# Kernel tuning notes

Measured on AMD Instinct MI355X. Metric: run time of the kernel, lower is better.

Reference implementation:

```python
import jax, jax.numpy as jnp
import numpy as np

EMBED_DIM = 1024
NUM_HEADS = 16
HEAD_DIM = EMBED_DIM // NUM_HEADS
T_Q = 2048
T_K = 2048
B = 4
NEG_INF = -1e9


def setup_inputs() -> dict:
    key = jax.random.key(0)
    ks = jax.random.split(key, 8)
    q = jax.random.normal(ks[0], (T_Q, B, EMBED_DIM), dtype=jnp.float32)
    k = jax.random.normal(ks[1], (T_K, B, EMBED_DIM), dtype=jnp.float32)
    v = jax.random.normal(ks[2], (T_K, B, EMBED_DIM), dtype=jnp.float32)
    # True = padded key position (masked out)
    key_padding_mask = jax.random.randint(ks[3], (B, T_K), 0, 2).astype(jnp.bool_)
    # torch nn.Linear weights: shape (out, in), y = x @ W^T
    scale = 1.0 / np.sqrt(EMBED_DIM)
    Wq = jax.random.uniform(ks[4], (EMBED_DIM, EMBED_DIM), jnp.float32, -scale, scale)
    Wk = jax.random.uniform(ks[5], (EMBED_DIM, EMBED_DIM), jnp.float32, -scale, scale)
    Wv = jax.random.uniform(ks[6], (EMBED_DIM, EMBED_DIM), jnp.float32, -scale, scale)
    Wo = jax.random.uniform(ks[7], (EMBED_DIM, EMBED_DIM), jnp.float32, -scale, scale)
    return {"q": q, "k": k, "v": v, "key_padding_mask": key_padding_mask,
            "Wq": Wq, "Wk": Wk, "Wv": Wv, "Wo": Wo}


def _proj_split(W, x):
    # x: (T, B, E), W: (E, E) torch layout -> (B, H, T, d_k)
    T = x.shape[0]
    y = jnp.einsum('tbe,fe->tbf', x, W)
    return y.reshape(T, B, NUM_HEADS, HEAD_DIM).transpose(1, 2, 0, 3)


def reference(q, k, v, key_padding_mask, Wq, Wk, Wv, Wo):
    Q = _proj_split(Wq, q)  # (B, H, T_q, d_k)
    K = _proj_split(Wk, k)  # (B, H, T_k, d_k)
    V = _proj_split(Wv, v)  # (B, H, T_k, d_k)
    scores = jnp.einsum('bhqd,bhkd->bhqk', Q, K) / jnp.sqrt(
        jnp.asarray(HEAD_DIM, dtype=Q.dtype))
    scores = jnp.where(key_padding_mask[:, None, None, :], NEG_INF, scores)
    attn = jax.nn.softmax(scores, axis=-1)  # dropout p=0.0 -> identity
    out = jnp.einsum('bhqk,bhkd->bhqd', attn, V)  # (B, H, T_q, d_k)
    out = out.transpose(2, 0, 1, 3).reshape(q.shape[0], q.shape[1], EMBED_DIM)
    return jnp.einsum('tbe,fe->tbf', out, Wo)
```

## Files before the change

kernel.cpp:

```cpp
#include <hip/hip_runtime.h>
#include <stdint.h>

#define TSEQ 2048
#define NB   4
#define NH   16
#define HD   64
#define EMB  1024
#define ROWS (TSEQ*NB)

typedef __attribute__((ext_vector_type(8))) short bf16x8;
typedef __attribute__((ext_vector_type(4))) short bf16x4;
typedef __attribute__((ext_vector_type(4))) float f32x4;

__device__ __forceinline__ short f2bf(float x) {
    uint32_t u = __builtin_bit_cast(uint32_t, x);
    u += 0x7fffu + ((u >> 16) & 1u);
    return (short)(u >> 16);
}

__device__ __forceinline__ uint32_t pack2bf(float a, float b) {
    uint32_t ua = __builtin_bit_cast(uint32_t, a) + 0x8000u;
    uint32_t ub = __builtin_bit_cast(uint32_t, b) + 0x8000u;
    return (ua >> 16) | (ub & 0xffff0000u);
}

__device__ __forceinline__ void gld16(const void* g, void* l) {
    __builtin_amdgcn_global_load_lds(
        (const __attribute__((address_space(1))) void*)g,
        (__attribute__((address_space(3))) void*)l,
        16, 0, 0);
}

__global__ __launch_bounds__(256)
void prep_kernel(const float* __restrict__ q, const float* __restrict__ k, const float* __restrict__ v,
                 const float* __restrict__ Wq, const float* __restrict__ Wk,
                 const float* __restrict__ Wv, const float* __restrict__ Wo,
                 short* __restrict__ Wbf,
                 short* __restrict__ Xq, short* __restrict__ Xk, short* __restrict__ Xv)
{
    int gid = blockIdx.x * 256 + threadIdx.x;
    const float4* s4;
    bf16x4* d4;
    if (gid < (1 << 20)) {
        int wsel = gid >> 18;
        const float* src = (wsel == 0) ? Wq : (wsel == 1) ? Wk : (wsel == 2) ? Wv : Wo;
        s4 = (const float4*)src + (gid & ((1 << 18) - 1));
        d4 = (bf16x4*)Wbf + gid;
    } else {
        int iid = gid - (1 << 20);
        int isel = iid >> 21, o = iid & ((1 << 21) - 1);
        const float* src = (isel == 0) ? q : (isel == 1) ? k : v;
        short* dst = (isel == 0) ? Xq : (isel == 1) ? Xk : Xv;
        s4 = (const float4*)src + o;
        d4 = (bf16x4*)dst + o;
    }
    float4 vv = *s4;
    bf16x4 o4 = { f2bf(vv.x), f2bf(vv.y), f2bf(vv.z), f2bf(vv.w) };
    *d4 = o4;
}

__global__ __launch_bounds__(256)
void scan_kernel(const int* __restrict__ mask, int* __restrict__ idxc,
                 float* __restrict__ bias_c, int* __restrict__ npad)
{
    const int b = blockIdx.x, tid = threadIdx.x;
    __shared__ int sums[256];
    __shared__ int totalv;
    const int* mb = mask + b * TSEQ;
    int valid[8]; int cnt = 0;
    #pragma unroll
    for (int j = 0; j < 8; j++) { valid[j] = (mb[tid * 8 + j] == 0); cnt += valid[j]; }
    sums[tid] = cnt;
    __syncthreads();
    for (int off = 1; off < 256; off <<= 1) {
        int vv = (tid >= off) ? sums[tid - off] : 0;
        __syncthreads();
        sums[tid] += vv;
        __syncthreads();
    }
    if (tid == 255) totalv = sums[255];
    int base = sums[tid] - cnt;
    __syncthreads();
    int nv = totalv;
    #pragma unroll
    for (int j = 0; j < 8; j++)
        if (valid[j]) { idxc[b * TSEQ + base] = tid * 8 + j; base++; }
    for (int i = tid; i < TSEQ; i += 256) {
        if (i >= nv) idxc[b * TSEQ + i] = 0;
        bias_c[b * TSEQ + i] = (i < nv) ? -12.0f : -1e9f;
    }
    if (tid == 0) npad[b] = (nv + 63) & ~63;
}

__global__ __launch_bounds__(256, 2)
void proj_gemm(const short* __restrict__ Xq, const short* __restrict__ Xk, const short* __restrict__ Xv,
               const short* __restrict__ Wbf,
               short* __restrict__ Qw, short* __restrict__ Kw, short* __restrict__ Vw)
{
    __shared__ __align__(16) short As[128*32];
    __shared__ __align__(16) short Bs[128*32];
    const int z = blockIdx.z;
    const short* __restrict__ A  = (z == 0) ? Xq : (z == 1) ? Xk : Xv;
    const short* __restrict__ Bw = Wbf + (size_t)z * (EMB*EMB);
    short* __restrict__ dst = (z == 0) ? Qw : (z == 1) ? Kw : Vw;
    const float scale = (z == 0) ? 0.18033688011112042f : 1.0f;

    const int tid = threadIdx.x;
    const int lane = tid & 63, w = tid >> 6;
    const int wm = w >> 1, wn = w & 1;
    const int g = lane >> 4, c = lane & 15;
    const int m0 = blockIdx.x * 128, n0 = blockIdx.y * 128;

    const int l4 = lane >> 2, col8 = (lane & 3) * 8;
    const short* gA = A  + (size_t)(m0 + w*16 + l4) * EMB + col8;
    const short* gB = Bw + (size_t)(n0 + w*16 + l4) * EMB + col8;
    short* ldsA0 = &As[(w*16) * 32];
    short* ldsA1 = &As[(64 + w*16) * 32];
    short* ldsB0 = &Bs[(w*16) * 32];
    short* ldsB1 = &Bs[(64 + w*16) * 32];

    f32x4 acc[4][4] = {};

    for (int kt = 0; kt < EMB; kt += 32) {
        gld16(gA + kt,            ldsA0);
        gld16(gA + 64*EMB + kt,   ldsA1);
        gld16(gB + kt,            ldsB0);
        gld16(gB + 64*EMB + kt,   ldsB1);
        __syncthreads();
        bf16x8 a[4], b[4];
        #pragma unroll
        for (int mt = 0; mt < 4; mt++) a[mt] = *(const bf16x8*)(&As[(wm*64 + mt*16 + c) * 32 + g * 8]);
        #pragma unroll
        for (int nt = 0; nt < 4; nt++) b[nt] = *(const bf16x8*)(&Bs[(wn*64 + nt*16 + c) * 32 + g * 8]);
        #pragma unroll
        for (int mt = 0; mt < 4; mt++)
            #pragma unroll
            for (int nt = 0; nt < 4; nt++)
                acc[mt][nt] = __builtin_amdgcn_mfma_f32_16x16x32_bf16(a[mt], b[nt], acc[mt][nt], 0, 0, 0);
        __syncthreads();
    }
    #pragma unroll
    for (int mt = 0; mt < 4; mt++)
        #pragma unroll
        for (int nt = 0; nt < 4; nt++)
            #pragma unroll
            for (int r = 0; r < 4; r++) {
                int row = m0 + wm*64 + mt*16 + g*4 + r;
                int col = n0 + wn*64 + nt*16 + c;
                int t = row >> 2, bb = row & 3, h = col >> 6, dk = col & 63;
                dst[(((size_t)(bb*16 + h) * TSEQ + t) << 6) + dk] = f2bf(acc[mt][nt][r] * scale);
            }
}

__global__ __launch_bounds__(256)
void gather_kv(const short* __restrict__ K, const short* __restrict__ V,
               const int* __restrict__ idxc, const int* __restrict__ npad,
               short* __restrict__ Kc, short* __restrict__ Vtc)
{
    const int bh = blockIdx.y, b = bh >> 4;
    const int i0 = blockIdx.x * 64;
    if (i0 >= npad[b]) return;
    __shared__ __align__(16) short tile[64*72];
    __shared__ int sidx[64];
    const int tid = threadIdx.x;
    if (tid < 64) sidx[tid] = idxc[b * TSEQ + i0 + tid];
    __syncthreads();
    const short* __restrict__ Kh = K + (size_t)bh * TSEQ * HD;
    const short* __restrict__ Vh = V + (size_t)bh * TSEQ * HD;
    #pragma unroll
    for (int p = 0; p < 2; p++) {
        int idx = tid + p * 256, row = idx >> 3, cc = idx & 7;
        int src = sidx[row];
        *(int4*)(Kc + ((size_t)bh * TSEQ + i0 + row) * HD + cc * 8)
            = *(const int4*)(Kh + (size_t)src * HD + cc * 8);
        *(int4*)(&tile[row * 72 + cc * 8]) = *(const int4*)(Vh + (size_t)src * HD + cc * 8);
    }
    __syncthreads();
    #pragma unroll
    for (int p = 0; p < 2; p++) {
        int idx = tid + p * 256, dv = idx >> 3, cc = idx & 7;
        bf16x8 o;
        #pragma unroll
        for (int j = 0; j < 8; j++) o[j] = tile[(cc * 8 + j) * 72 + dv];
        *(bf16x8*)(Vtc + ((size_t)bh * HD + dv) * TSEQ + i0 + cc * 8) = o;
    }
}

__global__ __launch_bounds__(256, 3)
void attn_kernel(const short* __restrict__ Q, const short* __restrict__ K,
                 const short* __restrict__ Vt, const float* __restrict__ bias,
                 const int* __restrict__ npad,
                 short* __restrict__ O)
{
    __shared__ __align__(16) short Ks [64*72];
    __shared__ __align__(16) short Vts[64*72];
    __shared__ __align__(16) short Ps [128*72];
    __shared__ __align__(16) float bias_lds[64];

    const int bh = blockIdx.y;
    const int b_ = bh >> 4, h_ = bh & 15;
    const int q0 = blockIdx.x * 128;
    const int tid = threadIdx.x, lane = tid & 63, wv = tid >> 6;
    const int g = lane >> 4, c = lane & 15;
    const int qb = wv * 32;
    const short* __restrict__ Qh  = Q  + (size_t)bh * TSEQ * HD;
    const short* __restrict__ Kh  = K  + (size_t)bh * TSEQ * HD;
    const short* __restrict__ Vth = Vt + (size_t)bh * HD * TSEQ;
    const float* __restrict__ biasb = bias + b_ * TSEQ;
    const int nit = npad[b_] >> 6;

    const int srow = tid >> 3, scc = tid & 7;

    *(int4*)(&Ks [ srow       * 72 + scc * 8]) = *(const int4*)(Kh  + (size_t) srow       * HD + scc * 8);
    *(int4*)(&Ks [(srow + 32) * 72 + scc * 8]) = *(const int4*)(Kh  + (size_t)(srow + 32) * HD + scc * 8);
    *(int4*)(&Vts[ srow       * 72 + scc * 8]) = *(const int4*)(Vth + (size_t) srow       * TSEQ + scc * 8);
    *(int4*)(&Vts[(srow + 32) * 72 + scc * 8]) = *(const int4*)(Vth + (size_t)(srow + 32) * TSEQ + scc * 8);
    if (tid < 16) ((float4*)bias_lds)[tid] = ((const float4*)biasb)[tid];

    bf16x8 qf[2][2];
    #pragma unroll
    for (int j = 0; j < 2; j++)
        #pragma unroll
        for (int ks = 0; ks < 2; ks++)
            qf[j][ks] = *(const bf16x8*)(Qh + (size_t)(q0 + qb + j * 16 + c) * HD + ks * 32 + g * 8);
    __syncthreads();

    float lacc[2] = { 0.0f, 0.0f };
    f32x4 oacc[2][4] = {};

    for (int it = 0; it < nit; it++) {
        f32x4 sacc[2][4];
        #pragma unroll
        for (int mt = 0; mt < 4; mt++) {
            f32x4 bv = *(const f32x4*)(&bias_lds[mt * 16 + g * 4]);
            sacc[0][mt] = bv; sacc[1][mt] = bv;
        }

        int4 kr0, kr1, vr0, vr1; float4 br;
        const bool pfv = (it + 1 < nit);
        if (pfv) {
            int tk0n = (it + 1) * 64;
            kr0 = *(const int4*)(Kh  + (size_t)(tk0n + srow)      * HD + scc * 8);
            kr1 = *(const int4*)(Kh  + (size_t)(tk0n + srow + 32) * HD + scc * 8);
            vr0 = *(const int4*)(Vth + (size_t) srow       * TSEQ + tk0n + scc * 8);
            vr1 = *(const int4*)(Vth + (size_t)(srow + 32) * TSEQ + tk0n + scc * 8);
            if (tid < 16) br = ((const float4*)(biasb + tk0n))[tid];
        }

        #pragma unroll
        for (int ks = 0; ks < 2; ks++)
            #pragma unroll
            for (int mt = 0; mt < 4; mt++) {
                bf16x8 kf = *(const bf16x8*)(&Ks[(mt * 16 + c) * 72 + ks * 32 + g * 8]);
                sacc[0][mt] = __builtin_amdgcn_mfma_f32_16x16x32_bf16(kf, qf[0][ks], sacc[0][mt], 0, 0, 0);
                sacc[1][mt] = __builtin_amdgcn_mfma_f32_16x16x32_bf16(kf, qf[1][ks], sacc[1][mt], 0, 0, 0);
            }

        #pragma unroll
        for (int j = 0; j < 2; j++) {
            int prow = (qb + j * 16 + c) * 72;
            float lp = 0.0f;
            #pragma unroll
            for (int mt = 0; mt < 4; mt++) {
                float e0 = __builtin_amdgcn_exp2f(sacc[j][mt][0]);
                float e1 = __builtin_amdgcn_exp2f(sacc[j][mt][1]);
                float e2 = __builtin_amdgcn_exp2f(sacc[j][mt][2]);
                float e3 = __builtin_amdgcn_exp2f(sacc[j][mt][3]);
                lp += (e0 + e1) + (e2 + e3);
                uint2 pw = { pack2bf(e0, e1), pack2bf(e2, e3) };
                *(uint2*)(&Ps[prow + mt * 16 + g * 4]) = pw;
            }
            lacc[j] += lp;
        }
        __builtin_amdgcn_sched_barrier(0);

        #pragma unroll
        for (int s2 = 0; s2 < 2; s2++) {
            bf16x8 pf0 = *(const bf16x8*)(&Ps[(qb +      c) * 72 + s2 * 32 + g * 8]);
            bf16x8 pf1 = *(const bf16x8*)(&Ps[(qb + 16 + c) * 72 + s2 * 32 + g * 8]);
            #pragma unroll
            for (int mtv = 0; mtv < 4; mtv++) {
                bf16x8 vf = *(const bf16x8*)(&Vts[(mtv * 16 + c) * 72 + s2 * 32 + g * 8]);
                oacc[0][mtv] = __builtin_amdgcn_mfma_f32_16x16x32_bf16(vf, pf0, oacc[0][mtv], 0, 0, 0);
                oacc[1][mtv] = __builtin_amdgcn_mfma_f32_16x16x32_bf16(vf, pf1, oacc[1][mtv], 0, 0, 0);
            }
        }

        if (pfv) {
            __syncthreads();
            *(int4*)(&Ks [ srow       * 72 + scc * 8]) = kr0;
            *(int4*)(&Ks [(srow + 32) * 72 + scc * 8]) = kr1;
            *(int4*)(&Vts[ srow       * 72 + scc * 8]) = vr0;
            *(int4*)(&Vts[(srow + 32) * 72 + scc * 8]) = vr1;
            if (tid < 16) ((float4*)bias_lds)[tid] = br;
            __syncthreads();
        }
    }

    __syncthreads();
    #pragma unroll
    for (int j = 0; j < 2; j++) {
        float l = lacc[j];
        l += __shfl_xor(l, 16);
        l += __shfl_xor(l, 32);
        float inv = 1.0f / l;
        int orow = (qb + j * 16 + c) * 72;
        #pragma unroll
        for (int mtv = 0; mtv < 4; mtv++) {
            uint2 ow = { pack2bf(oacc[j][mtv][0] * inv, oacc[j][mtv][1] * inv),
                         pack2bf(oacc[j][mtv][2] * inv, oacc[j][mtv][3] * inv) };
            *(uint2*)(&Ps[orow + mtv * 16 + g * 4]) = ow;
        }
    }
    __syncthreads();
    #pragma unroll
    for (int i = 0; i < 4; i++) {
        int idx = tid + i * 256, row = idx >> 3, cc = idx & 7;
        *(int4*)(O + (((size_t)(q0 + row) * NB + b_) << 10) + h_ * 64 + cc * 8)
            = *(const int4*)(&Ps[row * 72 + cc * 8]);
    }
}

__global__ __launch_bounds__(256, 2)
void out_gemm(const short* __restrict__ A, const short* __restrict__ Bw, float* __restrict__ C)
{
    __shared__ __align__(16) short As[128*32];
    __shared__ __align__(16) short Bs[128*32];
    const int tid = threadIdx.x;
    const int lane = tid & 63, w = tid >> 6;
    const int wm = w >> 1, wn = w & 1;
    const int g = lane >> 4, c = lane & 15;
    const int m0 = blockIdx.x * 128, n0 = blockIdx.y * 128;

    const int l4 = lane >> 2, col8 = (lane & 3) * 8;
    const short* gA = A  + (size_t)(m0 + w*16 + l4) * EMB + col8;
    const short* gB = Bw + (size_t)(n0 + w*16 + l4) * EMB + col8;
    short* ldsA0 = &As[(w*16) * 32];
    short* ldsA1 = &As[(64 + w*16) * 32];
    short* ldsB0 = &Bs[(w*16) * 32];
    short* ldsB1 = &Bs[(64 + w*16) * 32];

    f32x4 acc[4][4] = {};
    for (int kt = 0; kt < EMB; kt += 32) {
        gld16(gA + kt,          ldsA0);
        gld16(gA + 64*EMB + kt, ldsA1);
        gld16(gB + kt,          ldsB0);
        gld16(gB + 64*EMB + kt, ldsB1);
        __syncthreads();
        bf16x8 a[4], b[4];
        #pragma unroll
        for (int mt = 0; mt < 4; mt++) a[mt] = *(const bf16x8*)(&As[(wm*64 + mt*16 + c) * 32 + g * 8]);
        #pragma unroll
        for (int nt = 0; nt < 4; nt++) b[nt] = *(const bf16x8*)(&Bs[(wn*64 + nt*16 + c) * 32 + g * 8]);
        #pragma unroll
        for (int mt = 0; mt < 4; mt++)
            #pragma unroll
            for (int nt = 0; nt < 4; nt++)
                acc[mt][nt] = __builtin_amdgcn_mfma_f32_16x16x32_bf16(a[mt], b[nt], acc[mt][nt], 0, 0, 0);
        __syncthreads();
    }
    #pragma unroll
    for (int mt = 0; mt < 4; mt++)
        #pragma unroll
        for (int nt = 0; nt < 4; nt++)
            #pragma unroll
            for (int r = 0; r < 4; r++) {
                int row = m0 + wm*64 + mt*16 + g*4 + r;
                int col = n0 + wn*64 + nt*16 + c;
                C[(size_t)row * EMB + col] = acc[mt][nt][r];
            }
}

extern "C" void kernel_launch(void* const* d_in, const int* in_sizes, int n_in,
                              void* d_out, int out_size, void* d_ws, size_t ws_size,
                              hipStream_t stream)
{
    const float* q    = (const float*)d_in[0];
    const float* k    = (const float*)d_in[1];
    const float* v    = (const float*)d_in[2];
    const int*   mask = (const int*)  d_in[3];
    const float* Wq   = (const float*)d_in[4];
    const float* Wk   = (const float*)d_in[5];
    const float* Wv   = (const float*)d_in[6];
    const float* Wo   = (const float*)d_in[7];
    float* out = (float*)d_out;

    char* ws = (char*)d_ws;
    short* Wbf    = (short*)(ws);
    short* Qws    = (short*)(ws +  8388608);
    short* Kws    = (short*)(ws + 25165824);
    short* Vws    = (short*)(ws + 41943040);
    short* Vtc    = (short*)(ws + 58720256);
    short* Ows    = (short*)(ws + 75497472);
    float* bias_c = (float*)(ws + 92274688);
    short* Xvbf   = (short*)(ws + 92307456);
    int*   idxc   = (int*)  (ws + 109084672);
    int*   npad   = (int*)  (ws + 109117440);
    short* Xqbf = Ows;
    short* Xkbf = Vtc;
    short* Kc   = Xvbf;

    prep_kernel<<<28672, 256, 0, stream>>>(q, k, v, Wq, Wk, Wv, Wo, Wbf, Xqbf, Xkbf, Xvbf);
    scan_kernel<<<NB, 256, 0, stream>>>(mask, idxc, bias_c, npad);
    proj_gemm<<<dim3(ROWS/128, EMB/128, 3), 256, 0, stream>>>(Xqbf, Xkbf, Xvbf, Wbf, Qws, Kws, Vws);
    gather_kv<<<dim3(TSEQ/64, NB*NH), 256, 0, stream>>>(Kws, Vws, idxc, npad, Kc, Vtc);
    attn_kernel<<<dim3(TSEQ/128, NB*NH), 256, 0, stream>>>(Qws, Kc, Vtc, bias_c, npad, Ows);
    out_gemm<<<dim3(ROWS/128, EMB/128), 256, 0, stream>>>(Ows, Wbf + (size_t)3*EMB*EMB, out);
}
```

Baseline: 313.7 us.

## Rewrite QKV projection GEMM as 256x256 eight-wave pipelined kernel with swizzled LDS

Replaces the 128x128 four-wave projection GEMM with a 256x256 tile, 512-thread kernel. It uses a K-step of 64 with double-buffered LDS and XOR-swizzled layout, and splits each K-step into four quarter-tile phases that interleave global-to-LDS loads with MFMA work. Explicit barriers, waitcnt and setprio are used to overlap memory with compute. The aim is better data reuse and hiding of load latency, at the cost of larger LDS use (128KB per block) and fewer blocks (384) across the GPU.

```diff
diff --git a/kernel.cpp b/kernel.cpp
--- a/kernel.cpp
+++ b/kernel.cpp
@@ -7,6 +7,7 @@
 #define HD   64
 #define EMB  1024
 #define ROWS (TSEQ*NB)
+#define NKT  (EMB/64)
 
 typedef __attribute__((ext_vector_type(8))) short bf16x8;
 typedef __attribute__((ext_vector_type(4))) short bf16x4;
@@ -92,13 +93,59 @@
     if (tid == 0) npad[b] = (nv + 63) & ~63;
 }
 
-__global__ __launch_bounds__(256, 2)
-void proj_gemm(const short* __restrict__ Xq, const short* __restrict__ Xk, const short* __restrict__ Xv,
-               const short* __restrict__ Wbf,
-               short* __restrict__ Qw, short* __restrict__ Kw, short* __restrict__ Vw)
-{
-    __shared__ __align__(16) short As[128*32];
-    __shared__ __align__(16) short Bs[128*32];
+
+#define VMWAIT4 asm volatile("s_waitcnt vmcnt(4)" ::: "memory")
+
+#define PH(MH, NH, WAITSTMT, ...)                                                   \
+    {                                                                               \
+        const short* ah = &lds[cur][0][MH][0];                                      \
+        const short* bh = &lds[cur][1][NH][0];                                      \
+        bf16x8 af[4][2], bfr[2][2];                                                 \
+        _Pragma("unroll")                                                           \
+        for (int mf = 0; mf < 4; mf++) {                                            \
+            _Pragma("unroll")                                                       \
+            for (int ks = 0; ks < 2; ks++) {                                        \
+                const int rr = wm*64 + mf*16 + c;                                   \
+                const int cb = (ks*64 + g*16) ^ ((rr & 7) << 4);                    \
+                af[mf][ks] = *(const bf16x8*)(ah + rr*64 + (cb >> 1));              \
+            }                                                                       \
+        }                                                                           \
+        _Pragma("unroll")                                                           \
+        for (int nf = 0; nf < 2; nf++) {                                            \
+            _Pragma("unroll")                                                       \
+            for (int ks = 0; ks < 2; ks++) {                                        \
+                const int rr = wn*32 + nf*16 + c;                                   \
+                const int cb = (ks*64 + g*16) ^ ((rr & 7) << 4);                    \
+                bfr[nf][ks] = *(const bf16x8*)(bh + rr*64 + (cb >> 1));             \
+            }                                                                       \
+        }                                                                           \
+        __VA_ARGS__;                                                                \
+        __builtin_amdgcn_s_barrier();                                               \
+        asm volatile("s_waitcnt lgkmcnt(0)" ::: "memory");                          \
+        __builtin_amdgcn_sched_barrier(0);                                          \
+        __builtin_amdgcn_s_setprio(1);                                              \
+        _Pragma("unroll")                                                           \
+        for (int mf = 0; mf < 4; mf++) {                                            \
+            _Pragma("unroll")                                                       \
+            for (int nf = 0; nf < 2; nf++) {                                        \
+                acc[MH][NH][mf][nf] = __builtin_amdgcn_mfma_f32_16x16x32_bf16(      \
+                    af[mf][0], bfr[nf][0], acc[MH][NH][mf][nf], 0, 0, 0);           \
+                acc[MH][NH][mf][nf] = __builtin_amdgcn_mfma_f32_16x16x32_bf16(      \
+                    af[mf][1], bfr[nf][1], acc[MH][NH][mf][nf], 0, 0, 0);           \
+            }                                                                       \
+        }                                                                           \
+        __builtin_amdgcn_s_setprio(0);                                              \
+        __builtin_amdgcn_sched_barrier(0);                                          \
+        WAITSTMT;                                                                   \
+        __builtin_amdgcn_s_barrier();                                               \
+    }
+
+__global__ __launch_bounds__(512, 2)
+void proj_gemm8(const short* __restrict__ Xq, const short* __restrict__ Xk, const short* __restrict__ Xv,
+                const short* __restrict__ Wbf,
+                short* __restrict__ Qw, short* __restrict__ Kw, short* __restrict__ Vw)
+{
+    __shared__ __align__(16) short lds[2][2][2][128*64];
     const int z = blockIdx.z;
     const short* __restrict__ A  = (z == 0) ? Xq : (z == 1) ? Xk : Xv;
     const short* __restrict__ Bw = Wbf + (size_t)z * (EMB*EMB);
@@ -107,49 +154,64 @@
 
     const int tid = threadIdx.x;
     const int lane = tid & 63, w = tid >> 6;
-    const int wm = w >> 1, wn = w & 1;
+    const int wm = w >> 2, wn = w & 3;
     const int g = lane >> 4, c = lane & 15;
-    const int m0 = blockIdx.x * 128, n0 = blockIdx.y * 128;
-
-    const int l4 = lane >> 2, col8 = (lane & 3) * 8;
-    const short* gA = A  + (size_t)(m0 + w*16 + l4) * EMB + col8;
-    const short* gB = Bw + (size_t)(n0 + w*16 + l4) * EMB + col8;
-    short* ldsA0 = &As[(w*16) * 32];
-    short* ldsA1 = &As[(64 + w*16) * 32];
-    short* ldsB0 = &Bs[(w*16) * 32];
-    short* ldsB1 = &Bs[(64 + w*16) * 32];
-
-    f32x4 acc[4][4] = {};
-
-    for (int kt = 0; kt < EMB; kt += 32) {
-        gld16(gA + kt,            ldsA0);
-        gld16(gA + 64*EMB + kt,   ldsA1);
-        gld16(gB + kt,            ldsB0);
-        gld16(gB + 64*EMB + kt,   ldsB1);
-        __syncthreads();
-        bf16x8 a[4], b[4];
-        #pragma unroll
-        for (int mt = 0; mt < 4; mt++) a[mt] = *(const bf16x8*)(&As[(wm*64 + mt*16 + c) * 32 + g * 8]);
-        #pragma unroll
-        for (int nt = 0; nt < 4; nt++) b[nt] = *(const bf16x8*)(&Bs[(wn*64 + nt*16 + c) * 32 + g * 8]);
-        #pragma unroll
-        for (int mt = 0; mt < 4; mt++)
-            #pragma unroll
-            for (int nt = 0; nt < 4; nt++)
-                acc[mt][nt] = __builtin_amdgcn_mfma_f32_16x16x32_bf16(a[mt], b[nt], acc[mt][nt], 0, 0, 0);
-        __syncthreads();
-    }
-    #pragma unroll
-    for (int mt = 0; mt < 4; mt++)
-        #pragma unroll
-        for (int nt = 0; nt < 4; nt++)
-            #pragma unroll
-            for (int r = 0; r < 4; r++) {
-                int row = m0 + wm*64 + mt*16 + g*4 + r;
-                int col = n0 + wn*64 + nt*16 + c;
-                int t = row >> 2, bb = row & 3, h = col >> 6, dk = col & 63;
-                dst[(((size_t)(bb*16 + h) * TSEQ + t) << 6) + dk] = f2bf(acc[mt][nt][r] * scale);
-            }
+    const int m0 = blockIdx.x * 256, n0 = blockIdx.y * 256;
+
+    const short* a0 = A  + (size_t)m0 * EMB;
+    const short* a1 = a0 + (size_t)128 * EMB;
+    const short* b0 = Bw + (size_t)n0 * EMB;
+    const short* b1 = b0 + (size_t)128 * EMB;
+
+    auto stage = [&](const short* grow, short* lhalf) {
+        #pragma unroll
+        for (int p = 0; p < 2; p++) {
+            const int lin = p * 8192 + w * 1024 + lane * 16;
+            const int rin = lin >> 7;
+            const int cb  = (lin & 127) ^ ((rin & 7) << 4);
+            gld16(grow + (size_t)rin * EMB + (cb >> 1), lhalf + p * 4096 + w * 512);
+        }
+    };
+
+    stage(a0,      &lds[0][0][0][0]);
+    stage(a1,      &lds[0][0][1][0]);
+    stage(b0,      &lds[0][1][0][0]);
+    stage(b1,      &lds[0][1][1][0]);
+    stage(a0 + 64, &lds[1][0][0][0]);
+    stage(b0 + 64, &lds[1][1][0][0]);
+    VMWAIT4;
+    __builtin_amdgcn_s_barrier();
+
+    f32x4 acc[2][2][4][2] = {};
+
+    #pragma unroll 2
+    for (int t = 0; t < NKT; t++) {
+        const int cur = t & 1, nxt = cur ^ 1;
+        const int k1 = (t + 1 < NKT ? t + 1 : NKT - 1) * 64;
+        const int k2 = (t + 2 < NKT ? t + 2 : NKT - 1) * 64;
+        PH(0, 0, , stage(a1 + k1, &lds[nxt][0][1][0]))
+        PH(0, 1, , stage(b1 + k1, &lds[nxt][1][1][0]))
+        PH(1, 0, , stage(a0 + k2, &lds[cur][0][0][0]))
+        PH(1, 1, VMWAIT4, stage(b0 + k2, &lds[cur][1][0][0]))
+    }
+    asm volatile("s_waitcnt vmcnt(0)" ::: "memory");
+
+    #pragma unroll
+    for (int mh = 0; mh < 2; mh++)
+        #pragma unroll
+        for (int nh = 0; nh < 2; nh++)
+            #pragma unroll
+            for (int mf = 0; mf < 4; mf++)
+                #pragma unroll
+                for (int nf = 0; nf < 2; nf++)
+                    #pragma unroll
+                    for (int r = 0; r < 4; r++) {
+                        int row = m0 + mh*128 + wm*64 + mf*16 + g*4 + r;
+                        int col = n0 + nh*128 + wn*32 + nf*16 + c;
+                        int tq = row >> 2, bb = row & 3, h = col >> 6, dk = col & 63;
+                        dst[(((size_t)(bb*16 + h) * TSEQ + tq) << 6) + dk]
+                            = f2bf(acc[mh][nh][mf][nf][r] * scale);
+                    }
 }
 
 __global__ __launch_bounds__(256)
@@ -402,7 +464,7 @@
 
     prep_kernel<<<28672, 256, 0, stream>>>(q, k, v, Wq, Wk, Wv, Wo, Wbf, Xqbf, Xkbf, Xvbf);
     scan_kernel<<<NB, 256, 0, stream>>>(mask, idxc, bias_c, npad);
-    proj_gemm<<<dim3(ROWS/128, EMB/128, 3), 256, 0, stream>>>(Xqbf, Xkbf, Xvbf, Wbf, Qws, Kws, Vws);
+    proj_gemm8<<<dim3(ROWS/256, EMB/256, 3), 512, 0, stream>>>(Xqbf, Xkbf, Xvbf, Wbf, Qws, Kws, Vws);
     gather_kv<<<dim3(TSEQ/64, NB*NH), 256, 0, stream>>>(Kws, Vws, idxc, npad, Kc, Vtc);
     attn_kernel<<<dim3(TSEQ/128, NB*NH), 256, 0, stream>>>(Qws, Kc, Vtc, bias_c, npad, Ows);
     out_gemm<<<dim3(ROWS/128, EMB/128), 256, 0, stream>>>(Ows, Wbf + (size_t)3*EMB*EMB, out);
```

Measured after the change: 320.4 us. 1.02x slower.
